# Kernel optimization log

Measured on AMD Instinct MI355X. Metric: run time of the kernel, lower is better.

The kernel has to match this reference:

```python
import math
import jax, jax.numpy as jnp
import numpy as np

LENGTHS = [1024, 768, 512, 1024, 256, 896, 640, 512]  # ragged seq lens, sum = 5632
NEG = -10000.0  # mask fill value used by the torch module


def setup_inputs() -> dict:
    key = jax.random.key(0)
    k1, k2 = jax.random.split(key)
    total = int(sum(LENGTHS))  # 5632 packed tokens
    H, HKV, D = 16, 4, 64      # GQA: 16 query heads, 4 kv heads
    q = jax.random.normal(k1, (total, H, D), dtype=jnp.float32)
    kv = jax.random.normal(k2, (total, 2, HKV, D), dtype=jnp.float32)
    cu_seqlens = jnp.asarray(np.concatenate([[0], np.cumsum(LENGTHS)]), dtype=jnp.int32)
    return {"q": q, "kv": kv, "cu_seqlens": cu_seqlens, "max_seqlen": 1024}


def _varlen_attention(q, kv, cu_seqlens, max_seqlen):
    # GQA repeat: '... hkv d -> ... (hkv g) d' == repeat each kv head g times
    g = q.shape[1] // kv.shape[2]
    kv = jnp.repeat(kv, g, axis=2)
    k, v = kv[:, 0], kv[:, 1]            # [total, H, D]

    starts = cu_seqlens[:-1]
    lens = cu_seqlens[1:] - starts       # [B]
    S = max_seqlen
    pos = jnp.arange(S)
    gather_idx = starts[:, None] + pos[None, :]          # [B, S]
    key_mask = pos[None, :] < lens[:, None]              # [B, S] True = valid
    gather_idx = jnp.where(key_mask, gather_idx, 0)

    m = key_mask[:, :, None, None]
    # pad ragged tokens into dense [B, S, H, D] buffers (zeros where invalid)
    qp = jnp.where(m, q[gather_idx], 0.0)
    kp = jnp.where(m, k[gather_idx], 0.0)
    vp = jnp.where(m, v[gather_idx], 0.0)

    scale = 1.0 / math.sqrt(q.shape[-1])
    scores = jnp.einsum('bthd,bshd->bhts', qp, kp * scale)   # [B, H, S, S]
    # key padding mask: 0 on valid keys, -10000 on padded keys
    scores = scores + jnp.where(key_mask, 0.0, NEG)[:, None, None, :]
    # causal mask: triu(-10000, 1)
    scores = scores + jnp.triu(jnp.full((S, S), NEG, dtype=scores.dtype), 1)

    attn = jax.nn.softmax(scores, axis=-1)
    out_padded = jnp.einsum('bhts,bshd->bthd', attn, vp)     # [B, S, H, D]

    # unpad back to packed [total, H, D]
    tok = jnp.arange(q.shape[0])
    b = jnp.searchsorted(cu_seqlens, tok, side='right') - 1  # batch id per token
    s = tok - starts[b]                                      # position within seq
    return out_padded[b, s]


def reference(q, kv, cu_seqlens, max_seqlen):
    return _varlen_attention(q, kv, cu_seqlens, max_seqlen)
```

## Files before the change

### kernel.cpp

```cpp
#include <hip/hip_runtime.h>


#define H    16
#define HKV  4
#define D    64
#define BM   16
#define NEGF (-1e30f)

using bf8 = __attribute__((ext_vector_type(8))) short;
using f4v = __attribute__((ext_vector_type(4))) float;
typedef unsigned int u32;

union bf8u { bf8 v; u32 w[4]; };

__device__ inline u32 pk(float a, float b) {
    union { float f; u32 u; } x, y; x.f = a; y.f = b;
    return __builtin_amdgcn_perm(y.u + 0x8000u, x.u + 0x8000u, 0x07060302u);
}

#define MFMA(A, B, C) __builtin_amdgcn_mfma_f32_16x16x32_bf16(A, B, C, 0, 0, 0)

__global__ __launch_bounds__(256)
void preconv6(const float* __restrict__ kv, short* __restrict__ Kb,
              short* __restrict__ Vb, int ntiles)
{
    const int T = blockIdx.x, kvh = blockIdx.y, t = threadIdx.x;
    const int lane = t & 63, fi = t >> 6;
    const int qd = lane >> 4, c = lane & 15;
    const size_t tbase = ((size_t)kvh * ntiles + T) * 8;

    #pragma unroll
    for (int ff = 0; ff < 2; ++ff) {
        const int f = fi + 4 * ff;
        {
            const int ki = f >> 1, dc = f & 1;
            const int tok = 64 * T + ki * 16 + c;
            const float* p = kv + (size_t)tok * 512 + kvh * 64 + dc * 32 + qd * 8;
            float4 a = *(const float4*)p, b = *(const float4*)(p + 4);
            uint4 o = make_uint4(pk(a.x, a.y), pk(a.z, a.w), pk(b.x, b.y), pk(b.z, b.w));
            *(uint4*)&Kb[((tbase + f) * 64 + lane) * 8] = o;
        }
        {
            const int di = f >> 1, kc = f & 1;
            const int tok0 = 64 * T + kc * 32 + qd * 8;
            const float* p = kv + (size_t)tok0 * 512 + (HKV + kvh) * 64 + di * 16 + c;
            float v[8];
            #pragma unroll
            for (int j = 0; j < 8; ++j) v[j] = p[(size_t)j * 512];
            uint4 o = make_uint4(pk(v[0], v[1]), pk(v[2], v[3]), pk(v[4], v[5]), pk(v[6], v[7]));
            *(uint4*)&Vb[((tbase + f) * 64 + lane) * 8] = o;
        }
    }
}

__global__ __launch_bounds__(256, 4)
void attn6(const float* __restrict__ q, const short* __restrict__ Kb,
           const short* __restrict__ Vb, const int* __restrict__ cu,
           float* __restrict__ out, int nb, int ntiles)
{
    __shared__ __attribute__((aligned(16))) short Ps[4][BM * 72];

    const int kvh = blockIdx.y;

    int bid = blockIdx.x, b = -1, start = 0, len = 0, q0 = 0, acc = 0;
    for (int i = 0; i < nb; ++i) {
        int s0 = cu[i], l = cu[i + 1] - s0, nt = (l + BM - 1) / BM;
        if (bid < acc + nt) { b = i; start = s0; len = l; q0 = (nt - 1 - (bid - acc)) * BM; break; }
        acc += nt;
    }
    if (b < 0) return;

    const int t = threadIdx.x, w = t >> 6, lane = t & 63;
    const int qd = lane >> 4, c = lane & 15;
    const int h = kvh * 4 + w;
    const int rows = min(BM, len - q0), kend = q0 + rows;
    const int niter = (kend + 63) >> 6;
    const float SC = 0.125f * 1.44269504f;

    bf8u qf0, qf1;
    {
        int qr = min(c, rows - 1);
        const float* qp = q + (size_t)(start + q0 + qr) * (H * D) + h * D + qd * 8;
        float4 a0 = *(const float4*)qp;
        float4 a1 = *(const float4*)(qp + 4);
        float4 a2 = *(const float4*)(qp + 32);
        float4 a3 = *(const float4*)(qp + 36);
        qf0.w[0] = pk(a0.x * SC, a0.y * SC); qf0.w[1] = pk(a0.z * SC, a0.w * SC);
        qf0.w[2] = pk(a1.x * SC, a1.y * SC); qf0.w[3] = pk(a1.z * SC, a1.w * SC);
        qf1.w[0] = pk(a2.x * SC, a2.y * SC); qf1.w[1] = pk(a2.z * SC, a2.w * SC);
        qf1.w[2] = pk(a3.x * SC, a3.y * SC); qf1.w[3] = pk(a3.z * SC, a3.w * SC);
    }

    const size_t htile = (size_t)kvh * ntiles + (start >> 6);
    const short* kp0 = Kb + (htile * 8 * 64 + lane) * 8;
    const short* vp0 = Vb + (htile * 8 * 64 + lane) * 8;

    float l_i = 0.f;
    f4v o0 = {0,0,0,0}, o1 = {0,0,0,0}, o2 = {0,0,0,0}, o3 = {0,0,0,0};
    short* Psw = &Ps[w][0];

    for (int it = 0; it < niter; ++it) {
        const short* kp = kp0 + (size_t)it * 4096;
        const short* vp = vp0 + (size_t)it * 4096;

        bf8 kf[4][2], vf[4][2];
        #pragma unroll
        for (int ki = 0; ki < 4; ++ki) {
            kf[ki][0] = *(const bf8*)(kp + (ki * 2 + 0) * 512);
            kf[ki][1] = *(const bf8*)(kp + (ki * 2 + 1) * 512);
        }
        #pragma unroll
        for (int di = 0; di < 4; ++di) {
            vf[di][0] = *(const bf8*)(vp + (di * 2 + 0) * 512);
            vf[di][1] = *(const bf8*)(vp + (di * 2 + 1) * 512);
        }

        f4v s0 = {0,0,0,0}, s1 = {0,0,0,0}, s2 = {0,0,0,0}, s3 = {0,0,0,0};
        s0 = MFMA(kf[0][0], qf0.v, s0); s0 = MFMA(kf[0][1], qf1.v, s0);
        s1 = MFMA(kf[1][0], qf0.v, s1); s1 = MFMA(kf[1][1], qf1.v, s1);
        s2 = MFMA(kf[2][0], qf0.v, s2); s2 = MFMA(kf[2][1], qf1.v, s2);
        s3 = MFMA(kf[3][0], qf0.v, s3); s3 = MFMA(kf[3][1], qf1.v, s3);

        float e[16];
        #pragma unroll
        for (int r = 0; r < 4; ++r) {
            e[r] = s0[r]; e[4 + r] = s1[r]; e[8 + r] = s2[r]; e[12 + r] = s3[r];
        }
        const int kt0 = 64 * it;
        if (kt0 + 63 > q0) {
            const int limit = q0 + c - kt0;
            #pragma unroll
            for (int j = 0; j < 4; ++j)
                #pragma unroll
                for (int r = 0; r < 4; ++r)
                    if (16 * j + 4 * qd + r > limit) e[4 * j + r] = NEGF;
        }
        float ls = 0.f;
        #pragma unroll
        for (int i = 0; i < 16; ++i) { e[i] = exp2f(e[i]); ls += e[i]; }
        l_i += ls;

        #pragma unroll
        for (int j = 0; j < 4; ++j) {
            u32 lo = pk(e[4 * j], e[4 * j + 1]), hi = pk(e[4 * j + 2], e[4 * j + 3]);
            *(uint2*)&Psw[c * 72 + 16 * j + 4 * qd] = make_uint2(lo, hi);
        }
        bf8 p0 = *(const bf8*)&Psw[c * 72 + qd * 8];
        bf8 p1 = *(const bf8*)&Psw[c * 72 + 32 + qd * 8];

        o0 = MFMA(vf[0][0], p0, o0); o0 = MFMA(vf[0][1], p1, o0);
        o1 = MFMA(vf[1][0], p0, o1); o1 = MFMA(vf[1][1], p1, o1);
        o2 = MFMA(vf[2][0], p0, o2); o2 = MFMA(vf[2][1], p1, o2);
        o3 = MFMA(vf[3][0], p0, o3); o3 = MFMA(vf[3][1], p1, o3);
    }

    if (c < rows) {
        float lt = l_i + __shfl_xor(l_i, 16, 64);
        lt += __shfl_xor(lt, 32, 64);
        const float inv = 1.f / lt;
        float* op = out + (size_t)(start + q0 + c) * (H * D) + h * D + 4 * qd;
        *(float4*)(op)      = make_float4(o0[0] * inv, o0[1] * inv, o0[2] * inv, o0[3] * inv);
        *(float4*)(op + 16) = make_float4(o1[0] * inv, o1[1] * inv, o1[2] * inv, o1[3] * inv);
        *(float4*)(op + 32) = make_float4(o2[0] * inv, o2[1] * inv, o2[2] * inv, o2[3] * inv);
        *(float4*)(op + 48) = make_float4(o3[0] * inv, o3[1] * inv, o3[2] * inv, o3[3] * inv);
    }
}

extern "C" void kernel_launch(void* const* d_in, const int* in_sizes, int n_in,
                              void* d_out, int out_size, void* d_ws, size_t ws_size,
                              hipStream_t stream) {
    const float* q  = (const float*)d_in[0];
    const float* kv = (const float*)d_in[1];
    const int*   cu = (const int*)d_in[2];
    float* out = (float*)d_out;

    const int total  = in_sizes[0] / (H * D);
    const int nb     = in_sizes[2] - 1;
    const int ntiles = (total + 63) / 64;

    short* Kb = (short*)d_ws;
    short* Vb = Kb + (size_t)HKV * ntiles * 8 * 64 * 8;

    dim3 gridA(ntiles, HKV);
    preconv6<<<gridA, 256, 0, stream>>>(kv, Kb, Vb, ntiles);

    const int tile_ub = total / BM + nb;
    dim3 gridB(tile_ub, HKV);
    attn6<<<gridB, 256, 0, stream>>>(q, Kb, Vb, cu, out, nb, ntiles);
}
```

Baseline: 117.5 us.

## Process 32 query rows per block, prefetch K tiles, stage V transpose via LDS

Measured after the change: 117.5 us. About the same (+0.0%).

```diff
diff --git a/kernel.cpp b/kernel.cpp
--- a/kernel.cpp
+++ b/kernel.cpp
@@ -4,7 +4,7 @@
 #define H    16
 #define HKV  4
 #define D    64
-#define BM   16
+#define BM   32
 #define NEGF (-1e30f)
 
 using bf8 = __attribute__((ext_vector_type(8))) short;
@@ -21,44 +21,52 @@
 #define MFMA(A, B, C) __builtin_amdgcn_mfma_f32_16x16x32_bf16(A, B, C, 0, 0, 0)
 
 __global__ __launch_bounds__(256)
-void preconv6(const float* __restrict__ kv, short* __restrict__ Kb,
+void preconv7(const float* __restrict__ kv, short* __restrict__ Kb,
               short* __restrict__ Vb, int ntiles)
 {
+    __shared__ __attribute__((aligned(16))) float Vs[64 * 68];
+
     const int T = blockIdx.x, kvh = blockIdx.y, t = threadIdx.x;
     const int lane = t & 63, fi = t >> 6;
     const int qd = lane >> 4, c = lane & 15;
     const size_t tbase = ((size_t)kvh * ntiles + T) * 8;
 
     #pragma unroll
+    for (int i = 0; i < 4; ++i) {
+        int r = (t >> 4) + 16 * i, col = (t & 15) * 4;
+        float4 v = *(const float4*)&kv[(size_t)(64 * T + r) * 512 + (HKV + kvh) * 64 + col];
+        *(float4*)&Vs[r * 68 + col] = v;
+    }
+
+    #pragma unroll
     for (int ff = 0; ff < 2; ++ff) {
-        const int f = fi + 4 * ff;
-        {
-            const int ki = f >> 1, dc = f & 1;
-            const int tok = 64 * T + ki * 16 + c;
-            const float* p = kv + (size_t)tok * 512 + kvh * 64 + dc * 32 + qd * 8;
-            float4 a = *(const float4*)p, b = *(const float4*)(p + 4);
-            uint4 o = make_uint4(pk(a.x, a.y), pk(a.z, a.w), pk(b.x, b.y), pk(b.z, b.w));
-            *(uint4*)&Kb[((tbase + f) * 64 + lane) * 8] = o;
-        }
-        {
-            const int di = f >> 1, kc = f & 1;
-            const int tok0 = 64 * T + kc * 32 + qd * 8;
-            const float* p = kv + (size_t)tok0 * 512 + (HKV + kvh) * 64 + di * 16 + c;
-            float v[8];
-            #pragma unroll
-            for (int j = 0; j < 8; ++j) v[j] = p[(size_t)j * 512];
-            uint4 o = make_uint4(pk(v[0], v[1]), pk(v[2], v[3]), pk(v[4], v[5]), pk(v[6], v[7]));
-            *(uint4*)&Vb[((tbase + f) * 64 + lane) * 8] = o;
-        }
-    }
-}
-
-__global__ __launch_bounds__(256, 4)
-void attn6(const float* __restrict__ q, const short* __restrict__ Kb,
+        const int f = fi + 4 * ff, ki = f >> 1, dc = f & 1;
+        const int tok = 64 * T + ki * 16 + c;
+        const float* p = kv + (size_t)tok * 512 + kvh * 64 + dc * 32 + qd * 8;
+        float4 a = *(const float4*)p, b = *(const float4*)(p + 4);
+        uint4 o = make_uint4(pk(a.x, a.y), pk(a.z, a.w), pk(b.x, b.y), pk(b.z, b.w));
+        *(uint4*)&Kb[((tbase + f) * 64 + lane) * 8] = o;
+    }
+
+    __syncthreads();
+
+    #pragma unroll
+    for (int ff = 0; ff < 2; ++ff) {
+        const int f = fi + 4 * ff, di = f >> 1, kc = f & 1;
+        float v[8];
+        #pragma unroll
+        for (int j = 0; j < 8; ++j) v[j] = Vs[(kc * 32 + qd * 8 + j) * 68 + di * 16 + c];
+        uint4 o = make_uint4(pk(v[0], v[1]), pk(v[2], v[3]), pk(v[4], v[5]), pk(v[6], v[7]));
+        *(uint4*)&Vb[((tbase + f) * 64 + lane) * 8] = o;
+    }
+}
+
+__global__ __launch_bounds__(256, 2)
+void attn7(const float* __restrict__ q, const short* __restrict__ Kb,
            const short* __restrict__ Vb, const int* __restrict__ cu,
            float* __restrict__ out, int nb, int ntiles)
 {
-    __shared__ __attribute__((aligned(16))) short Ps[4][BM * 72];
+    __shared__ __attribute__((aligned(16))) short Ps[4][2 * BM / 2 * 72];
 
     const int kvh = blockIdx.y;
 
@@ -77,92 +85,124 @@
     const int niter = (kend + 63) >> 6;
     const float SC = 0.125f * 1.44269504f;
 
-    bf8u qf0, qf1;
-    {
-        int qr = min(c, rows - 1);
+    bf8u qf[2][2];
+    #pragma unroll
+    for (int s = 0; s < 2; ++s) {
+        int qr = min(16 * s + c, rows - 1);
         const float* qp = q + (size_t)(start + q0 + qr) * (H * D) + h * D + qd * 8;
         float4 a0 = *(const float4*)qp;
         float4 a1 = *(const float4*)(qp + 4);
         float4 a2 = *(const float4*)(qp + 32);
         float4 a3 = *(const float4*)(qp + 36);
-        qf0.w[0] = pk(a0.x * SC, a0.y * SC); qf0.w[1] = pk(a0.z * SC, a0.w * SC);
-        qf0.w[2] = pk(a1.x * SC, a1.y * SC); qf0.w[3] = pk(a1.z * SC, a1.w * SC);
-        qf1.w[0] = pk(a2.x * SC, a2.y * SC); qf1.w[1] = pk(a2.z * SC, a2.w * SC);
-        qf1.w[2] = pk(a3.x * SC, a3.y * SC); qf1.w[3] = pk(a3.z * SC, a3.w * SC);
+        qf[s][0].w[0] = pk(a0.x * SC, a0.y * SC); qf[s][0].w[1] = pk(a0.z * SC, a0.w * SC);
+        qf[s][0].w[2] = pk(a1.x * SC, a1.y * SC); qf[s][0].w[3] = pk(a1.z * SC, a1.w * SC);
+        qf[s][1].w[0] = pk(a2.x * SC, a2.y * SC); qf[s][1].w[1] = pk(a2.z * SC, a2.w * SC);
+        qf[s][1].w[2] = pk(a3.x * SC, a3.y * SC); qf[s][1].w[3] = pk(a3.z * SC, a3.w * SC);
     }
 
     const size_t htile = (size_t)kvh * ntiles + (start >> 6);
     const short* kp0 = Kb + (htile * 8 * 64 + lane) * 8;
     const short* vp0 = Vb + (htile * 8 * 64 + lane) * 8;
 
-    float l_i = 0.f;
-    f4v o0 = {0,0,0,0}, o1 = {0,0,0,0}, o2 = {0,0,0,0}, o3 = {0,0,0,0};
+    float l_i[2] = {0.f, 0.f};
+    f4v o[2][4];
+    #pragma unroll
+    for (int s = 0; s < 2; ++s)
+        #pragma unroll
+        for (int d = 0; d < 4; ++d) o[s][d] = (f4v){0, 0, 0, 0};
+
     short* Psw = &Ps[w][0];
 
+    bf8 kc_[4][2];
+    #pragma unroll
+    for (int ki = 0; ki < 4; ++ki) {
+        kc_[ki][0] = *(const bf8*)(kp0 + (ki * 2 + 0) * 512);
+        kc_[ki][1] = *(const bf8*)(kp0 + (ki * 2 + 1) * 512);
+    }
+
     for (int it = 0; it < niter; ++it) {
-        const short* kp = kp0 + (size_t)it * 4096;
         const short* vp = vp0 + (size_t)it * 4096;
-
-        bf8 kf[4][2], vf[4][2];
-        #pragma unroll
-        for (int ki = 0; ki < 4; ++ki) {
-            kf[ki][0] = *(const bf8*)(kp + (ki * 2 + 0) * 512);
-            kf[ki][1] = *(const bf8*)(kp + (ki * 2 + 1) * 512);
-        }
+        bf8 vf[4][2];
         #pragma unroll
         for (int di = 0; di < 4; ++di) {
             vf[di][0] = *(const bf8*)(vp + (di * 2 + 0) * 512);
             vf[di][1] = *(const bf8*)(vp + (di * 2 + 1) * 512);
         }
-
-        f4v s0 = {0,0,0,0}, s1 = {0,0,0,0}, s2 = {0,0,0,0}, s3 = {0,0,0,0};
-        s0 = MFMA(kf[0][0], qf0.v, s0); s0 = MFMA(kf[0][1], qf1.v, s0);
-        s1 = MFMA(kf[1][0], qf0.v, s1); s1 = MFMA(kf[1][1], qf1.v, s1);
-        s2 = MFMA(kf[2][0], qf0.v, s2); s2 = MFMA(kf[2][1], qf1.v, s2);
-        s3 = MFMA(kf[3][0], qf0.v, s3); s3 = MFMA(kf[3][1], qf1.v, s3);
-
-        float e[16];
-        #pragma unroll
-        for (int r = 0; r < 4; ++r) {
-            e[r] = s0[r]; e[4 + r] = s1[r]; e[8 + r] = s2[r]; e[12 + r] = s3[r];
-        }
+        const short* kp = kp0 + (size_t)min(it + 1, niter - 1) * 4096;
+        bf8 kn_[4][2];
+        #pragma unroll
+        for (int ki = 0; ki < 4; ++ki) {
+            kn_[ki][0] = *(const bf8*)(kp + (ki * 2 + 0) * 512);
+            kn_[ki][1] = *(const bf8*)(kp + (ki * 2 + 1) * 512);
+        }
+
+        f4v s0[4], s1[4];
+        #pragma unroll
+        for (int ki = 0; ki < 4; ++ki) {
+            f4v z = {0, 0, 0, 0};
+            z = MFMA(kc_[ki][0], qf[0][0].v, z);
+            s0[ki] = MFMA(kc_[ki][1], qf[0][1].v, z);
+            f4v y = {0, 0, 0, 0};
+            y = MFMA(kc_[ki][0], qf[1][0].v, y);
+            s1[ki] = MFMA(kc_[ki][1], qf[1][1].v, y);
+        }
+
         const int kt0 = 64 * it;
-        if (kt0 + 63 > q0) {
-            const int limit = q0 + c - kt0;
+        bf8 p[2][2];
+        #pragma unroll
+        for (int s = 0; s < 2; ++s) {
+            float e[16];
             #pragma unroll
-            for (int j = 0; j < 4; ++j)
+            for (int ki = 0; ki < 4; ++ki)
                 #pragma unroll
                 for (int r = 0; r < 4; ++r)
-                    if (16 * j + 4 * qd + r > limit) e[4 * j + r] = NEGF;
-        }
-        float ls = 0.f;
-        #pragma unroll
-        for (int i = 0; i < 16; ++i) { e[i] = exp2f(e[i]); ls += e[i]; }
-        l_i += ls;
-
-        #pragma unroll
-        for (int j = 0; j < 4; ++j) {
-            u32 lo = pk(e[4 * j], e[4 * j + 1]), hi = pk(e[4 * j + 2], e[4 * j + 3]);
-            *(uint2*)&Psw[c * 72 + 16 * j + 4 * qd] = make_uint2(lo, hi);
-        }
-        bf8 p0 = *(const bf8*)&Psw[c * 72 + qd * 8];
-        bf8 p1 = *(const bf8*)&Psw[c * 72 + 32 + qd * 8];
-
-        o0 = MFMA(vf[0][0], p0, o0); o0 = MFMA(vf[0][1], p1, o0);
-        o1 = MFMA(vf[1][0], p0, o1); o1 = MFMA(vf[1][1], p1, o1);
-        o2 = MFMA(vf[2][0], p0, o2); o2 = MFMA(vf[2][1], p1, o2);
-        o3 = MFMA(vf[3][0], p0, o3); o3 = MFMA(vf[3][1], p1, o3);
-    }
-
-    if (c < rows) {
-        float lt = l_i + __shfl_xor(l_i, 16, 64);
-        lt += __shfl_xor(lt, 32, 64);
-        const float inv = 1.f / lt;
-        float* op = out + (size_t)(start + q0 + c) * (H * D) + h * D + 4 * qd;
-        *(float4*)(op)      = make_float4(o0[0] * inv, o0[1] * inv, o0[2] * inv, o0[3] * inv);
-        *(float4*)(op + 16) = make_float4(o1[0] * inv, o1[1] * inv, o1[2] * inv, o1[3] * inv);
-        *(float4*)(op + 32) = make_float4(o2[0] * inv, o2[1] * inv, o2[2] * inv, o2[3] * inv);
-        *(float4*)(op + 48) = make_float4(o3[0] * inv, o3[1] * inv, o3[2] * inv, o3[3] * inv);
+                    e[4 * ki + r] = s ? s1[ki][r] : s0[ki][r];
+            if (kt0 + 63 > q0 + 16 * s) {
+                const int limit = q0 + 16 * s + c - kt0;
+                #pragma unroll
+                for (int ki = 0; ki < 4; ++ki)
+                    #pragma unroll
+                    for (int r = 0; r < 4; ++r)
+                        if (16 * ki + 4 * qd + r > limit) e[4 * ki + r] = NEGF;
+            }
+            float ls = 0.f;
+            #pragma unroll
+            for (int i = 0; i < 16; ++i) { e[i] = exp2f(e[i]); ls += e[i]; }
+            l_i[s] += ls;
+            short* Pss = Psw + s * 16 * 72;
+            #pragma unroll
+            for (int j = 0; j < 4; ++j) {
+                u32 lo = pk(e[4 * j], e[4 * j + 1]), hi = pk(e[4 * j + 2], e[4 * j + 3]);
+                *(uint2*)&Pss[c * 72 + 16 * j + 4 * qd] = make_uint2(lo, hi);
+            }
+            p[s][0] = *(const bf8*)&Pss[c * 72 + qd * 8];
+            p[s][1] = *(const bf8*)&Pss[c * 72 + 32 + qd * 8];
+        }
+
+        #pragma unroll
+        for (int di = 0; di < 4; ++di) {
+            o[0][di] = MFMA(vf[di][0], p[0][0], o[0][di]);
+            o[0][di] = MFMA(vf[di][1], p[0][1], o[0][di]);
+            o[1][di] = MFMA(vf[di][0], p[1][0], o[1][di]);
+            o[1][di] = MFMA(vf[di][1], p[1][1], o[1][di]);
+        }
+
+        #pragma unroll
+        for (int ki = 0; ki < 4; ++ki) { kc_[ki][0] = kn_[ki][0]; kc_[ki][1] = kn_[ki][1]; }
+    }
+
+    #pragma unroll
+    for (int s = 0; s < 2; ++s) {
+        if (16 * s + c < rows) {
+            float lt = l_i[s] + __shfl_xor(l_i[s], 16, 64);
+            lt += __shfl_xor(lt, 32, 64);
+            const float inv = 1.f / lt;
+            float* op = out + (size_t)(start + q0 + 16 * s + c) * (H * D) + h * D + 4 * qd;
+            *(float4*)(op)      = make_float4(o[s][0][0] * inv, o[s][0][1] * inv, o[s][0][2] * inv, o[s][0][3] * inv);
+            *(float4*)(op + 16) = make_float4(o[s][1][0] * inv, o[s][1][1] * inv, o[s][1][2] * inv, o[s][1][3] * inv);
+            *(float4*)(op + 32) = make_float4(o[s][2][0] * inv, o[s][2][1] * inv, o[s][2][2] * inv, o[s][2][3] * inv);
+            *(float4*)(op + 48) = make_float4(o[s][3][0] * inv, o[s][3][1] * inv, o[s][3][2] * inv, o[s][3][3] * inv);
+        }
     }
 }
 
@@ -182,9 +222,9 @@
     short* Vb = Kb + (size_t)HKV * ntiles * 8 * 64 * 8;
 
     dim3 gridA(ntiles, HKV);
-    preconv6<<<gridA, 256, 0, stream>>>(kv, Kb, Vb, ntiles);
+    preconv7<<<gridA, 256, 0, stream>>>(kv, Kb, Vb, ntiles);
 
     const int tile_ub = total / BM + nb;
     dim3 gridB(tile_ub, HKV);
-    attn6<<<gridB, 256, 0, stream>>>(q, Kb, Vb, cu, out, nb, ntiles);
-}
+    attn7<<<gridB, 256, 0, stream>>>(q, Kb, Vb, cu, out, nb, ntiles);
+}
```
